# Kernel tuning notes

Measured on AMD Instinct MI355X. Metric: run time of the kernel, lower is better.

The kernel has to match this reference:

```python
import jax, jax.numpy as jnp
import numpy as np

TEMPERATURE = 0.5


def setup_inputs() -> dict:
    key = jax.random.key(0)
    k1, k2 = jax.random.split(key)
    N, D = 4096, 256
    z_i = jax.random.normal(k1, (N, D), dtype=jnp.float32)
    z_j = jax.random.normal(k2, (N, D), dtype=jnp.float32)
    return {"z_i": z_i, "z_j": z_j}


def reference(z_i, z_j):
    N = z_i.shape[0]
    z = jnp.concatenate([z_i, z_j], axis=0)            # (2N, D)
    sim = (z @ z.T) / TEMPERATURE                       # (2N, 2N)
    # mask self-similarity on the diagonal
    diag = jnp.eye(2 * N, dtype=bool)
    sim = jnp.where(diag, -jnp.inf, sim)
    # positive pair labels: i <-> i+N
    labels = jnp.concatenate([jnp.arange(N, 2 * N), jnp.arange(0, N)])
    logp = jax.nn.log_softmax(sim, axis=-1)             # (2N, 2N)
    loss = -jnp.mean(jnp.take_along_axis(logp, labels[:, None], axis=-1))
    return loss
```

## Files before the change

kernel.cpp:

```cpp
#include <hip/hip_runtime.h>
#include <hip/hip_bf16.h>


typedef __bf16 bf16x8 __attribute__((ext_vector_type(8)));
typedef __bf16 bf16x4 __attribute__((ext_vector_type(4)));
typedef float  f32x16 __attribute__((ext_vector_type(16)));

#define NPAIR 4096
#define NROW  8192
#define DIM   256
#define STRIPS 16
#define RBLK  16384
#define SQSCALE 1.6986437f
#define LN2F    0.6931471805599453f
#define M2      176.0f

#define EXP2F(x) __builtin_amdgcn_exp2f(x)

__global__ __launch_bounds__(256) void k_convert(const float* __restrict__ zi,
                                                 const float* __restrict__ zj,
                                                 __bf16* __restrict__ Zf,
                                                 float* __restrict__ pos,
                                                 float* __restrict__ out) {
    const int w = threadIdx.x >> 6, lane = threadIdx.x & 63;
    const int r = blockIdx.x * 4 + w;
    if (blockIdx.x == 0 && threadIdx.x == 0) out[0] = 0.0f;
    const float4 vi = *(const float4*)(zi + r * DIM + lane * 4);
    const float4 vj = *(const float4*)(zj + r * DIM + lane * 4);
    bf16x4 bi, bj;
    bi[0] = (__bf16)(vi.x * SQSCALE); bi[1] = (__bf16)(vi.y * SQSCALE);
    bi[2] = (__bf16)(vi.z * SQSCALE); bi[3] = (__bf16)(vi.w * SQSCALE);
    bj[0] = (__bf16)(vj.x * SQSCALE); bj[1] = (__bf16)(vj.y * SQSCALE);
    bj[2] = (__bf16)(vj.z * SQSCALE); bj[3] = (__bf16)(vj.w * SQSCALE);
    const int t = lane >> 2, h = (lane >> 1) & 1, inner = (lane & 1) * 8;
    char* Zb = (char*)Zf;
    *(bf16x4*)(Zb + (size_t)(r >> 5) * RBLK + t * 1024 + h * 512 + (r & 31) * 16 + inner) = bi;
    const int r2 = r + NPAIR;
    *(bf16x4*)(Zb + (size_t)(r2 >> 5) * RBLK + t * 1024 + h * 512 + (r2 & 31) * 16 + inner) = bj;
    float d = vi.x * vj.x + vi.y * vj.y + vi.z * vj.z + vi.w * vj.w;
    #pragma unroll
    for (int m = 32; m >= 1; m >>= 1) d += __shfl_xor(d, m);
    if (lane == 0) pos[r] = 2.0f * d;
}

__global__ __launch_bounds__(64, 2) void k_lse(const __bf16* __restrict__ Zf,
                                               float* __restrict__ Lpart) {
    const int bid    = blockIdx.x;
    const int strip  = bid >> 7;
    const int rowblk = bid & 127;
    const int lane = threadIdx.x & 63, lm = lane & 31, half = lane >> 5;
    const int laneoff = half * 512 + lm * 16;
    const int R0 = rowblk * 2, R1 = R0 + 1;

    const char* Zb = (const char*)Zf;

    const char* g0 = Zb + (size_t)R0 * RBLK + laneoff;
    const char* g1 = Zb + (size_t)R1 * RBLK + laneoff;
    #define LOADB(i) \
        bf16x8 B0_##i = *(const bf16x8*)(g0 + (i) * 1024); \
        bf16x8 B1_##i = *(const bf16x8*)(g1 + (i) * 1024);
    LOADB(0)  LOADB(1)  LOADB(2)  LOADB(3)
    LOADB(4)  LOADB(5)  LOADB(6)  LOADB(7)
    LOADB(8)  LOADB(9)  LOADB(10) LOADB(11)
    LOADB(12) LOADB(13) LOADB(14) LOADB(15)
    #undef LOADB

    const char* Ap = Zb + (size_t)strip * 16 * RBLK + laneoff;

    bf16x8 A0 = *(const bf16x8*)(Ap + 0 * 1024);
    bf16x8 A1 = *(const bf16x8*)(Ap + 1 * 1024);
    bf16x8 A2 = *(const bf16x8*)(Ap + 2 * 1024);
    bf16x8 A3 = *(const bf16x8*)(Ap + 3 * 1024);

    float l0 = 0.0f, l1 = 0.0f;

    #define RSTEP(i, RN) {                                                         \
        bf16x8 a_ = RN;                                                            \
        RN = *(const bf16x8*)(At + ((i) + 4) * 1024);                              \
        acc0 = __builtin_amdgcn_mfma_f32_32x32x16_bf16(a_, B0_##i, acc0, 0, 0, 0); \
        acc1 = __builtin_amdgcn_mfma_f32_32x32x16_bf16(a_, B1_##i, acc1, 0, 0, 0); \
    }

    for (int tile = 0; tile < 16; ++tile) {
        const char* At = Ap + (size_t)tile * RBLK;
        f32x16 acc0 = (f32x16)(0.0f);
        f32x16 acc1 = (f32x16)(0.0f);
        __builtin_amdgcn_s_setprio(1);
        RSTEP(0,  A0) RSTEP(1,  A1) RSTEP(2,  A2) RSTEP(3,  A3)
        RSTEP(4,  A0) RSTEP(5,  A1) RSTEP(6,  A2) RSTEP(7,  A3)
        RSTEP(8,  A0) RSTEP(9,  A1) RSTEP(10, A2) RSTEP(11, A3)
        RSTEP(12, A0) RSTEP(13, A1) RSTEP(14, A2) RSTEP(15, A3)
        __builtin_amdgcn_s_setprio(0);

        const int cb = strip * 16 + tile;
        if (cb == R0) {
            #pragma unroll
            for (int rg = 0; rg < 16; rg++) {
                const int cl = (rg & 3) + 8 * (rg >> 2) + 4 * half;
                acc0[rg] = (cl == lm) ? -1e30f : acc0[rg];
            }
        }
        if (cb == R1) {
            #pragma unroll
            for (int rg = 0; rg < 16; rg++) {
                const int cl = (rg & 3) + 8 * (rg >> 2) + 4 * half;
                acc1[rg] = (cl == lm) ? -1e30f : acc1[rg];
            }
        }
        float p0 = 0.0f, p1 = 0.0f, q0 = 0.0f, q1 = 0.0f;
        #pragma unroll
        for (int rg = 0; rg < 16; rg += 2) {
            p0 += EXP2F(acc0[rg]     - M2);
            p1 += EXP2F(acc0[rg + 1] - M2);
            q0 += EXP2F(acc1[rg]     - M2);
            q1 += EXP2F(acc1[rg + 1] - M2);
        }
        l0 += p0 + p1;
        l1 += q0 + q1;
    }
    #undef RSTEP

    l0 += __shfl_xor(l0, 32);
    l1 += __shfl_xor(l1, 32);
    if (half == 0) {
        Lpart[strip * NROW + R0 * 32 + lm] = l0;
        Lpart[strip * NROW + R1 * 32 + lm] = l1;
    }
}

__global__ __launch_bounds__(256) void k_final(const float* __restrict__ Lpart,
                                               const float* __restrict__ pos,
                                               float* __restrict__ out) {
    __shared__ float red[256];
    const int t = threadIdx.x;
    const int r = blockIdx.x * 256 + t;
    float l = 0.0f;
    #pragma unroll
    for (int s = 0; s < STRIPS; s++) l += Lpart[s * NROW + r];
    const float lse = (M2 + __builtin_log2f(l)) * LN2F;
    red[t] = lse - pos[r & (NPAIR - 1)];
    __syncthreads();
    for (int ofs = 128; ofs > 0; ofs >>= 1) {
        if (t < ofs) red[t] += red[t + ofs];
        __syncthreads();
    }
    if (t == 0) atomicAdd(out, red[0] / (float)NROW);
}

extern "C" void kernel_launch(void* const* d_in, const int* in_sizes, int n_in,
                              void* d_out, int out_size, void* d_ws, size_t ws_size,
                              hipStream_t stream) {
    const float* zi = (const float*)d_in[0];
    const float* zj = (const float*)d_in[1];
    __bf16* Zf   = (__bf16*)d_ws;
    float* pos   = (float*)((char*)d_ws + (size_t)NROW * DIM * 2);
    float* Lpart = pos + NPAIR;

    k_convert<<<NPAIR / 4, 256, 0, stream>>>(zi, zj, Zf, pos, (float*)d_out);
    k_lse<<<128 * STRIPS, 64, 0, stream>>>(Zf, Lpart);
    k_final<<<NROW / 256, 256, 0, stream>>>(Lpart, pos, (float*)d_out);
}
```

Measured before the change: 102.4 us.

## Switch LSE kernel to 16x16x32 MFMA tiles with batched A prefetch

Replaces the 32x32x16 bf16 MFMA tiling in the log-sum-exp kernel with 16x16x32 MFMAs over a 4x2 grid of 16x16 accumulator blocks per tile. B operands are kept in registers as 32 fragments, and A fragments are double-buffered in two sets with explicit vmcnt waits and sched barriers between batches of 16 MFMAs. The diagonal masking and the exp2 reduction are rewritten for the new accumulator layout. The aim is better MFMA throughput and overlap of loads with compute, at the cost of hand-tuned scheduling and a layout-dependent masking scheme that could be wrong if the lane mapping is off.

```diff
diff --git a/kernel.cpp b/kernel.cpp
--- a/kernel.cpp
+++ b/kernel.cpp
@@ -4,7 +4,7 @@
 
 typedef __bf16 bf16x8 __attribute__((ext_vector_type(8)));
 typedef __bf16 bf16x4 __attribute__((ext_vector_type(4)));
-typedef float  f32x16 __attribute__((ext_vector_type(16)));
+typedef float  f32x4  __attribute__((ext_vector_type(4)));
 
 #define NPAIR 4096
 #define NROW  8192
@@ -48,83 +48,101 @@
     const int bid    = blockIdx.x;
     const int strip  = bid >> 7;
     const int rowblk = bid & 127;
-    const int lane = threadIdx.x & 63, lm = lane & 31, half = lane >> 5;
-    const int laneoff = half * 512 + lm * 16;
-    const int R0 = rowblk * 2, R1 = R0 + 1;
+    const int lane = threadIdx.x & 63;
+    const int l4 = lane >> 4;
+    const int laneoff16 = (l4 >> 1) * 1024 + (l4 & 1) * 512 + (lane & 15) * 16;
 
     const char* Zb = (const char*)Zf;
 
-    const char* g0 = Zb + (size_t)R0 * RBLK + laneoff;
-    const char* g1 = Zb + (size_t)R1 * RBLK + laneoff;
-    #define LOADB(i) \
-        bf16x8 B0_##i = *(const bf16x8*)(g0 + (i) * 1024); \
-        bf16x8 B1_##i = *(const bf16x8*)(g1 + (i) * 1024);
-    LOADB(0)  LOADB(1)  LOADB(2)  LOADB(3)
-    LOADB(4)  LOADB(5)  LOADB(6)  LOADB(7)
-    LOADB(8)  LOADB(9)  LOADB(10) LOADB(11)
-    LOADB(12) LOADB(13) LOADB(14) LOADB(15)
+    #define LOADB(RT, KC) \
+        bf16x8 B_##RT##_##KC = *(const bf16x8*)(Zb + \
+            (size_t)(rowblk * 2 + ((RT) >> 1)) * RBLK + (KC) * 2048 + \
+            ((RT) & 1) * 256 + laneoff16);
+    LOADB(0,0) LOADB(0,1) LOADB(0,2) LOADB(0,3) LOADB(0,4) LOADB(0,5) LOADB(0,6) LOADB(0,7)
+    LOADB(1,0) LOADB(1,1) LOADB(1,2) LOADB(1,3) LOADB(1,4) LOADB(1,5) LOADB(1,6) LOADB(1,7)
+    LOADB(2,0) LOADB(2,1) LOADB(2,2) LOADB(2,3) LOADB(2,4) LOADB(2,5) LOADB(2,6) LOADB(2,7)
+    LOADB(3,0) LOADB(3,1) LOADB(3,2) LOADB(3,3) LOADB(3,4) LOADB(3,5) LOADB(3,6) LOADB(3,7)
     #undef LOADB
 
-    const char* Ap = Zb + (size_t)strip * 16 * RBLK + laneoff;
+    const char* Ap = Zb + (size_t)strip * 16 * RBLK + laneoff16;
 
-    bf16x8 A0 = *(const bf16x8*)(Ap + 0 * 1024);
-    bf16x8 A1 = *(const bf16x8*)(Ap + 1 * 1024);
-    bf16x8 A2 = *(const bf16x8*)(Ap + 2 * 1024);
-    bf16x8 A3 = *(const bf16x8*)(Ap + 3 * 1024);
+    bf16x8 P0 = *(const bf16x8*)(Ap + 0);
+    bf16x8 P1 = *(const bf16x8*)(Ap + 256);
+    bf16x8 P2 = *(const bf16x8*)(Ap + 2048);
+    bf16x8 P3 = *(const bf16x8*)(Ap + 2304);
+    bf16x8 Q0 = *(const bf16x8*)(Ap + 4096);
+    bf16x8 Q1 = *(const bf16x8*)(Ap + 4352);
+    bf16x8 Q2 = *(const bf16x8*)(Ap + 6144);
+    bf16x8 Q3 = *(const bf16x8*)(Ap + 6400);
 
-    float l0 = 0.0f, l1 = 0.0f;
+    f32x4 c00 = (f32x4)(0.0f), c01 = (f32x4)(0.0f);
+    f32x4 c10 = (f32x4)(0.0f), c11 = (f32x4)(0.0f);
+    f32x4 c20 = (f32x4)(0.0f), c21 = (f32x4)(0.0f);
+    f32x4 c30 = (f32x4)(0.0f), c31 = (f32x4)(0.0f);
+    float l_0 = 0.0f, l_1 = 0.0f, l_2 = 0.0f, l_3 = 0.0f;
 
-    #define RSTEP(i, RN) {                                                         \
-        bf16x8 a_ = RN;                                                            \
-        RN = *(const bf16x8*)(At + ((i) + 4) * 1024);                              \
-        acc0 = __builtin_amdgcn_mfma_f32_32x32x16_bf16(a_, B0_##i, acc0, 0, 0, 0); \
-        acc1 = __builtin_amdgcn_mfma_f32_32x32x16_bf16(a_, B1_##i, acc1, 0, 0, 0); \
+    #define MM(AF, RT, KC, CC) \
+        CC = __builtin_amdgcn_mfma_f32_16x16x32_bf16(AF, B_##RT##_##KC, CC, 0, 0, 0);
+
+    #define BATCH(S0, S1, S2, S3, KA, KB, REF) {                                   \
+        asm volatile("s_waitcnt vmcnt(4)" ::: "memory");                           \
+        __builtin_amdgcn_sched_barrier(0);                                         \
+        __builtin_amdgcn_s_setprio(1);                                             \
+        MM(S0, 0, KA, c00) MM(S0, 1, KA, c10) MM(S0, 2, KA, c20) MM(S0, 3, KA, c30)\
+        MM(S1, 0, KA, c01) MM(S1, 1, KA, c11) MM(S1, 2, KA, c21) MM(S1, 3, KA, c31)\
+        MM(S2, 0, KB, c00) MM(S2, 1, KB, c10) MM(S2, 2, KB, c20) MM(S2, 3, KB, c30)\
+        MM(S3, 0, KB, c01) MM(S3, 1, KB, c11) MM(S3, 2, KB, c21) MM(S3, 3, KB, c31)\
+        __builtin_amdgcn_s_setprio(0);                                             \
+        S0 = *(const bf16x8*)(At + (REF) + 0);                                     \
+        S1 = *(const bf16x8*)(At + (REF) + 256);                                   \
+        S2 = *(const bf16x8*)(At + (REF) + 2048);                                  \
+        S3 = *(const bf16x8*)(At + (REF) + 2304);                                  \
     }
+
+    const int rbase = rowblk * 64;
+    const bool dlane = ((lane & 15) >> 2) == l4;
+    const int dreg = lane & 3;
 
     for (int tile = 0; tile < 16; ++tile) {
         const char* At = Ap + (size_t)tile * RBLK;
-        f32x16 acc0 = (f32x16)(0.0f);
-        f32x16 acc1 = (f32x16)(0.0f);
-        __builtin_amdgcn_s_setprio(1);
-        RSTEP(0,  A0) RSTEP(1,  A1) RSTEP(2,  A2) RSTEP(3,  A3)
-        RSTEP(4,  A0) RSTEP(5,  A1) RSTEP(6,  A2) RSTEP(7,  A3)
-        RSTEP(8,  A0) RSTEP(9,  A1) RSTEP(10, A2) RSTEP(11, A3)
-        RSTEP(12, A0) RSTEP(13, A1) RSTEP(14, A2) RSTEP(15, A3)
-        __builtin_amdgcn_s_setprio(0);
 
-        const int cb = strip * 16 + tile;
-        if (cb == R0) {
-            #pragma unroll
-            for (int rg = 0; rg < 16; rg++) {
-                const int cl = (rg & 3) + 8 * (rg >> 2) + 4 * half;
-                acc0[rg] = (cl == lm) ? -1e30f : acc0[rg];
-            }
+        BATCH(P0, P1, P2, P3, 0, 1, 8192)
+        BATCH(Q0, Q1, Q2, Q3, 2, 3, 12288)
+        BATCH(P0, P1, P2, P3, 4, 5, 16384)
+        BATCH(Q0, Q1, Q2, Q3, 6, 7, 20480)
+
+        const int cbase = strip * 512 + tile * 32;
+        #define POISON(RT, CT, CC) \
+            if (cbase + (CT) * 16 == rbase + (RT) * 16 && dlane) CC[dreg] = -1e30f;
+        POISON(0,0,c00) POISON(0,1,c01) POISON(1,0,c10) POISON(1,1,c11)
+        POISON(2,0,c20) POISON(2,1,c21) POISON(3,0,c30) POISON(3,1,c31)
+        #undef POISON
+
+        #pragma unroll
+        for (int rg = 0; rg < 4; rg++) {
+            l_0 += EXP2F(c00[rg] - M2) + EXP2F(c01[rg] - M2);
+            l_1 += EXP2F(c10[rg] - M2) + EXP2F(c11[rg] - M2);
+            l_2 += EXP2F(c20[rg] - M2) + EXP2F(c21[rg] - M2);
+            l_3 += EXP2F(c30[rg] - M2) + EXP2F(c31[rg] - M2);
         }
-        if (cb == R1) {
-            #pragma unroll
-            for (int rg = 0; rg < 16; rg++) {
-                const int cl = (rg & 3) + 8 * (rg >> 2) + 4 * half;
-                acc1[rg] = (cl == lm) ? -1e30f : acc1[rg];
-            }
-        }
-        float p0 = 0.0f, p1 = 0.0f, q0 = 0.0f, q1 = 0.0f;
-        #pragma unroll
-        for (int rg = 0; rg < 16; rg += 2) {
-            p0 += EXP2F(acc0[rg]     - M2);
-            p1 += EXP2F(acc0[rg + 1] - M2);
-            q0 += EXP2F(acc1[rg]     - M2);
-            q1 += EXP2F(acc1[rg + 1] - M2);
-        }
-        l0 += p0 + p1;
-        l1 += q0 + q1;
+        c00 = (f32x4)(0.0f); c01 = (f32x4)(0.0f);
+        c10 = (f32x4)(0.0f); c11 = (f32x4)(0.0f);
+        c20 = (f32x4)(0.0f); c21 = (f32x4)(0.0f);
+        c30 = (f32x4)(0.0f); c31 = (f32x4)(0.0f);
     }
-    #undef RSTEP
+    #undef BATCH
+    #undef MM
 
-    l0 += __shfl_xor(l0, 32);
-    l1 += __shfl_xor(l1, 32);
-    if (half == 0) {
-        Lpart[strip * NROW + R0 * 32 + lm] = l0;
-        Lpart[strip * NROW + R1 * 32 + lm] = l1;
+    l_0 += __shfl_xor(l_0, 16); l_0 += __shfl_xor(l_0, 32);
+    l_1 += __shfl_xor(l_1, 16); l_1 += __shfl_xor(l_1, 32);
+    l_2 += __shfl_xor(l_2, 16); l_2 += __shfl_xor(l_2, 32);
+    l_3 += __shfl_xor(l_3, 16); l_3 += __shfl_xor(l_3, 32);
+    if (lane < 16) {
+        float* Lp = Lpart + strip * NROW + rbase + lane;
+        Lp[0]  = l_0;
+        Lp[16] = l_1;
+        Lp[32] = l_2;
+        Lp[48] = l_3;
     }
 }
 
```

Measured after the change: 96.73 us. 1.06x faster.

## Replace per-wave register-resident GEMM with LDS-tiled 256x256 block GEMM

Applied to the files above, without the earlier changes.

The similarity GEMM moves from 64-thread blocks that stream A fragments straight from global memory to 512-thread blocks computing 256x256 tiles. Those blocks stage swizzled K-slices into double-buffered LDS via global_load_lds and use 16x16x32 MFMAs. The packed bf16 layout becomes plain row-major, and the row-sum partials grow from 16 to 128 chunks, so the final reduction reads more data. The intent is more operand reuse and less global traffic, at the cost of LDS pressure, barriers and a heavier partial-sum reduction.

```diff
diff --git a/kernel.cpp b/kernel.cpp
--- a/kernel.cpp
+++ b/kernel.cpp
@@ -4,13 +4,12 @@
 
 typedef __bf16 bf16x8 __attribute__((ext_vector_type(8)));
 typedef __bf16 bf16x4 __attribute__((ext_vector_type(4)));
-typedef float  f32x16 __attribute__((ext_vector_type(16)));
+typedef float  f32x4  __attribute__((ext_vector_type(4)));
 
 #define NPAIR 4096
 #define NROW  8192
 #define DIM   256
-#define STRIPS 16
-#define RBLK  16384
+#define NCHUNK 128
 #define SQSCALE 1.6986437f
 #define LN2F    0.6931471805599453f
 #define M2      176.0f
@@ -19,7 +18,7 @@
 
 __global__ __launch_bounds__(256) void k_convert(const float* __restrict__ zi,
                                                  const float* __restrict__ zj,
-                                                 __bf16* __restrict__ Zf,
+                                                 __bf16* __restrict__ Zp,
                                                  float* __restrict__ pos,
                                                  float* __restrict__ out) {
     const int w = threadIdx.x >> 6, lane = threadIdx.x & 63;
@@ -32,100 +31,129 @@
     bi[2] = (__bf16)(vi.z * SQSCALE); bi[3] = (__bf16)(vi.w * SQSCALE);
     bj[0] = (__bf16)(vj.x * SQSCALE); bj[1] = (__bf16)(vj.y * SQSCALE);
     bj[2] = (__bf16)(vj.z * SQSCALE); bj[3] = (__bf16)(vj.w * SQSCALE);
-    const int t = lane >> 2, h = (lane >> 1) & 1, inner = (lane & 1) * 8;
-    char* Zb = (char*)Zf;
-    *(bf16x4*)(Zb + (size_t)(r >> 5) * RBLK + t * 1024 + h * 512 + (r & 31) * 16 + inner) = bi;
-    const int r2 = r + NPAIR;
-    *(bf16x4*)(Zb + (size_t)(r2 >> 5) * RBLK + t * 1024 + h * 512 + (r2 & 31) * 16 + inner) = bj;
+    char* Zb = (char*)Zp;
+    *(bf16x4*)(Zb + (size_t)r * 512 + lane * 8) = bi;
+    *(bf16x4*)(Zb + (size_t)(r + NPAIR) * 512 + lane * 8) = bj;
     float d = vi.x * vj.x + vi.y * vj.y + vi.z * vj.z + vi.w * vj.w;
     #pragma unroll
     for (int m = 32; m >= 1; m >>= 1) d += __shfl_xor(d, m);
     if (lane == 0) pos[r] = 2.0f * d;
 }
 
-__global__ __launch_bounds__(64, 2) void k_lse(const __bf16* __restrict__ Zf,
-                                               float* __restrict__ Lpart) {
-    const int bid    = blockIdx.x;
-    const int strip  = bid >> 7;
-    const int rowblk = bid & 127;
-    const int lane = threadIdx.x & 63, lm = lane & 31, half = lane >> 5;
-    const int laneoff = half * 512 + lm * 16;
-    const int R0 = rowblk * 2, R1 = R0 + 1;
+__global__ __launch_bounds__(512, 2) void k_lse(const __bf16* __restrict__ Zp,
+                                                float* __restrict__ Lpart) {
+    const int bid = blockIdx.x;
+    const int br = bid >> 5, bc = bid & 31;
+    const int tid = threadIdx.x;
+    const int w = tid >> 6, lane = tid & 63;
+    const int wr = w >> 2, wc = w & 3;
+    const int l15 = lane & 15, l4 = lane >> 4;
 
-    const char* Zb = (const char*)Zf;
+    __shared__ __align__(16) char smem[65536];
+    const char* Zb = (const char*)Zp;
+    const int arow0 = br * 256, brow0 = bc * 256;
 
-    const char* g0 = Zb + (size_t)R0 * RBLK + laneoff;
-    const char* g1 = Zb + (size_t)R1 * RBLK + laneoff;
-    #define LOADB(i) \
-        bf16x8 B0_##i = *(const bf16x8*)(g0 + (i) * 1024); \
-        bf16x8 B1_##i = *(const bf16x8*)(g1 + (i) * 1024);
-    LOADB(0)  LOADB(1)  LOADB(2)  LOADB(3)
-    LOADB(4)  LOADB(5)  LOADB(6)  LOADB(7)
-    LOADB(8)  LOADB(9)  LOADB(10) LOADB(11)
-    LOADB(12) LOADB(13) LOADB(14) LOADB(15)
-    #undef LOADB
+    const int j16sw = (l4 * 16) ^ ((lane & 3) << 4);
+    const int aBase = (wr * 128 + l15) * 64 + j16sw;
+    const int bBase = (wc * 64  + l15) * 64 + j16sw;
 
-    const char* Ap = Zb + (size_t)strip * 16 * RBLK + laneoff;
+    #define STAGE(KT) do {                                                           \
+        char* db = smem + ((KT) & 1) * 32768;                                        \
+        _Pragma("unroll")                                                            \
+        for (int q = 0; q < 2; q++) {                                                \
+            const int c = q * 512 + tid;                                             \
+            const int row = c >> 2;                                                  \
+            const int inner = ((c & 3) * 16) ^ ((row & 3) << 4);                     \
+            __builtin_amdgcn_global_load_lds(                                        \
+                (const __attribute__((address_space(1))) unsigned int*)              \
+                    (Zb + (size_t)(arow0 + row) * 512 + (KT) * 64 + inner),          \
+                (__attribute__((address_space(3))) unsigned int*)(db + c * 16),      \
+                16, 0, 0);                                                           \
+        }                                                                            \
+        _Pragma("unroll")                                                            \
+        for (int q = 0; q < 2; q++) {                                                \
+            const int c = q * 512 + tid;                                             \
+            const int row = c >> 2;                                                  \
+            const int inner = ((c & 3) * 16) ^ ((row & 3) << 4);                     \
+            __builtin_amdgcn_global_load_lds(                                        \
+                (const __attribute__((address_space(1))) unsigned int*)              \
+                    (Zb + (size_t)(brow0 + row) * 512 + (KT) * 64 + inner),          \
+                (__attribute__((address_space(3))) unsigned int*)(db + 16384 + c * 16), \
+                16, 0, 0);                                                           \
+        }                                                                            \
+    } while (0)
 
-    bf16x8 A0 = *(const bf16x8*)(Ap + 0 * 1024);
-    bf16x8 A1 = *(const bf16x8*)(Ap + 1 * 1024);
-    bf16x8 A2 = *(const bf16x8*)(Ap + 2 * 1024);
-    bf16x8 A3 = *(const bf16x8*)(Ap + 3 * 1024);
+    #define DECL(M) f32x4 c##M##0 = (f32x4)(0.0f), c##M##1 = (f32x4)(0.0f), \
+                          c##M##2 = (f32x4)(0.0f), c##M##3 = (f32x4)(0.0f);
+    DECL(0) DECL(1) DECL(2) DECL(3) DECL(4) DECL(5) DECL(6) DECL(7)
+    #undef DECL
 
-    float l0 = 0.0f, l1 = 0.0f;
+    STAGE(0);
+    STAGE(1);
 
-    #define RSTEP(i, RN) {                                                         \
-        bf16x8 a_ = RN;                                                            \
-        RN = *(const bf16x8*)(At + ((i) + 4) * 1024);                              \
-        acc0 = __builtin_amdgcn_mfma_f32_32x32x16_bf16(a_, B0_##i, acc0, 0, 0, 0); \
-        acc1 = __builtin_amdgcn_mfma_f32_32x32x16_bf16(a_, B1_##i, acc1, 0, 0, 0); \
+    #define MROW(M, AF) \
+        c##M##0 = __builtin_amdgcn_mfma_f32_16x16x32_bf16(AF, b0, c##M##0, 0, 0, 0); \
+        c##M##1 = __builtin_amdgcn_mfma_f32_16x16x32_bf16(AF, b1, c##M##1, 0, 0, 0); \
+        c##M##2 = __builtin_amdgcn_mfma_f32_16x16x32_bf16(AF, b2, c##M##2, 0, 0, 0); \
+        c##M##3 = __builtin_amdgcn_mfma_f32_16x16x32_bf16(AF, b3, c##M##3, 0, 0, 0);
+
+    for (int kt = 0; kt < 8; ++kt) {
+        if (kt < 7) { asm volatile("s_waitcnt vmcnt(4)" ::: "memory"); }
+        else        { asm volatile("s_waitcnt vmcnt(0)" ::: "memory"); }
+        __builtin_amdgcn_s_barrier();
+        const char* Ab = smem + (kt & 1) * 32768;
+        const char* Bb = Ab + 16384;
+        bf16x8 a0 = *(const bf16x8*)(Ab + aBase + 0 * 1024);
+        bf16x8 a1 = *(const bf16x8*)(Ab + aBase + 1 * 1024);
+        bf16x8 a2 = *(const bf16x8*)(Ab + aBase + 2 * 1024);
+        bf16x8 a3 = *(const bf16x8*)(Ab + aBase + 3 * 1024);
+        bf16x8 a4 = *(const bf16x8*)(Ab + aBase + 4 * 1024);
+        bf16x8 a5 = *(const bf16x8*)(Ab + aBase + 5 * 1024);
+        bf16x8 a6 = *(const bf16x8*)(Ab + aBase + 6 * 1024);
+        bf16x8 a7 = *(const bf16x8*)(Ab + aBase + 7 * 1024);
+        bf16x8 b0 = *(const bf16x8*)(Bb + bBase + 0 * 1024);
+        bf16x8 b1 = *(const bf16x8*)(Bb + bBase + 1 * 1024);
+        bf16x8 b2 = *(const bf16x8*)(Bb + bBase + 2 * 1024);
+        bf16x8 b3 = *(const bf16x8*)(Bb + bBase + 3 * 1024);
+        __builtin_amdgcn_s_setprio(1);
+        MROW(0, a0) MROW(1, a1) MROW(2, a2) MROW(3, a3)
+        MROW(4, a4) MROW(5, a5) MROW(6, a6) MROW(7, a7)
+        __builtin_amdgcn_s_setprio(0);
+        __builtin_amdgcn_s_barrier();
+        if (kt < 6) STAGE(kt + 2);
     }
+    #undef MROW
+    #undef STAGE
 
-    for (int tile = 0; tile < 16; ++tile) {
-        const char* At = Ap + (size_t)tile * RBLK;
-        f32x16 acc0 = (f32x16)(0.0f);
-        f32x16 acc1 = (f32x16)(0.0f);
-        __builtin_amdgcn_s_setprio(1);
-        RSTEP(0,  A0) RSTEP(1,  A1) RSTEP(2,  A2) RSTEP(3,  A3)
-        RSTEP(4,  A0) RSTEP(5,  A1) RSTEP(6,  A2) RSTEP(7,  A3)
-        RSTEP(8,  A0) RSTEP(9,  A1) RSTEP(10, A2) RSTEP(11, A3)
-        RSTEP(12, A0) RSTEP(13, A1) RSTEP(14, A2) RSTEP(15, A3)
-        __builtin_amdgcn_s_setprio(0);
+    const bool diagblk = (br == bc);
+    const bool dlane = (l15 >> 2) == l4;
+    const int dreg = lane & 3;
+    float* Lp = Lpart + (size_t)(bc * 4 + wc) * NROW + arow0 + wr * 128;
 
-        const int cb = strip * 16 + tile;
-        if (cb == R0) {
-            #pragma unroll
-            for (int rg = 0; rg < 16; rg++) {
-                const int cl = (rg & 3) + 8 * (rg >> 2) + 4 * half;
-                acc0[rg] = (cl == lm) ? -1e30f : acc0[rg];
-            }
-        }
-        if (cb == R1) {
-            #pragma unroll
-            for (int rg = 0; rg < 16; rg++) {
-                const int cl = (rg & 3) + 8 * (rg >> 2) + 4 * half;
-                acc1[rg] = (cl == lm) ? -1e30f : acc1[rg];
-            }
-        }
-        float p0 = 0.0f, p1 = 0.0f, q0 = 0.0f, q1 = 0.0f;
-        #pragma unroll
-        for (int rg = 0; rg < 16; rg += 2) {
-            p0 += EXP2F(acc0[rg]     - M2);
-            p1 += EXP2F(acc0[rg + 1] - M2);
-            q0 += EXP2F(acc1[rg]     - M2);
-            q1 += EXP2F(acc1[rg + 1] - M2);
-        }
-        l0 += p0 + p1;
-        l1 += q0 + q1;
+    #define EPIT(MT, NT) {                                                           \
+        f32x4 v = c##MT##NT;                                                         \
+        const bool dp = diagblk && dlane && (wr * 128 + (MT) * 16 == wc * 64 + (NT) * 16); \
+        r0 += EXP2F(((dp && dreg == 0) ? -1e30f : v[0]) - M2);                       \
+        r1 += EXP2F(((dp && dreg == 1) ? -1e30f : v[1]) - M2);                       \
+        r2 += EXP2F(((dp && dreg == 2) ? -1e30f : v[2]) - M2);                       \
+        r3 += EXP2F(((dp && dreg == 3) ? -1e30f : v[3]) - M2);                       \
     }
-    #undef RSTEP
-
-    l0 += __shfl_xor(l0, 32);
-    l1 += __shfl_xor(l1, 32);
-    if (half == 0) {
-        Lpart[strip * NROW + R0 * 32 + lm] = l0;
-        Lpart[strip * NROW + R1 * 32 + lm] = l1;
+    #define EPI(MT) {                                                                \
+        float r0 = 0.0f, r1 = 0.0f, r2 = 0.0f, r3 = 0.0f;                            \
+        EPIT(MT, 0) EPIT(MT, 1) EPIT(MT, 2) EPIT(MT, 3)                              \
+        r0 += __shfl_xor(r0, 1); r0 += __shfl_xor(r0, 2);                            \
+        r0 += __shfl_xor(r0, 4); r0 += __shfl_xor(r0, 8);                            \
+        r1 += __shfl_xor(r1, 1); r1 += __shfl_xor(r1, 2);                            \
+        r1 += __shfl_xor(r1, 4); r1 += __shfl_xor(r1, 8);                            \
+        r2 += __shfl_xor(r2, 1); r2 += __shfl_xor(r2, 2);                            \
+        r2 += __shfl_xor(r2, 4); r2 += __shfl_xor(r2, 8);                            \
+        r3 += __shfl_xor(r3, 1); r3 += __shfl_xor(r3, 2);                            \
+        r3 += __shfl_xor(r3, 4); r3 += __shfl_xor(r3, 8);                            \
+        if (l15 == 0) *(float4*)(Lp + (MT) * 16 + l4 * 4) = make_float4(r0, r1, r2, r3); \
     }
+    EPI(0) EPI(1) EPI(2) EPI(3) EPI(4) EPI(5) EPI(6) EPI(7)
+    #undef EPI
+    #undef EPIT
 }
 
 __global__ __launch_bounds__(256) void k_final(const float* __restrict__ Lpart,
@@ -135,8 +163,8 @@
     const int t = threadIdx.x;
     const int r = blockIdx.x * 256 + t;
     float l = 0.0f;
-    #pragma unroll
-    for (int s = 0; s < STRIPS; s++) l += Lpart[s * NROW + r];
+    #pragma unroll 8
+    for (int s = 0; s < NCHUNK; s++) l += Lpart[(size_t)s * NROW + r];
     const float lse = (M2 + __builtin_log2f(l)) * LN2F;
     red[t] = lse - pos[r & (NPAIR - 1)];
     __syncthreads();
@@ -152,11 +180,11 @@
                               hipStream_t stream) {
     const float* zi = (const float*)d_in[0];
     const float* zj = (const float*)d_in[1];
-    __bf16* Zf   = (__bf16*)d_ws;
+    __bf16* Zp   = (__bf16*)d_ws;
     float* pos   = (float*)((char*)d_ws + (size_t)NROW * DIM * 2);
     float* Lpart = pos + NPAIR;
 
-    k_convert<<<NPAIR / 4, 256, 0, stream>>>(zi, zj, Zf, pos, (float*)d_out);
-    k_lse<<<128 * STRIPS, 64, 0, stream>>>(Zf, Lpart);
+    k_convert<<<NPAIR / 4, 256, 0, stream>>>(zi, zj, Zp, pos, (float*)d_out);
+    k_lse<<<32 * 32, 512, 0, stream>>>(Zp, Lpart);
     k_final<<<NROW / 256, 256, 0, stream>>>(Lpart, pos, (float*)d_out);
 }
```

New measurement: 113.9 us. +11.2%, slower.
